# Kernel tuning notes

Hardware: AMD Instinct MI355X
Metric: run time of the kernel (lower is better)

## Reference

```python
import jax, jax.numpy as jnp
import numpy as np

H = 1024
V = 32000
S = 2048


def _lstm_cell(x, h_prev, c_prev, W_ih, W_hh, b_ih, b_hh):
    # PyTorch gate order: input, forget, cell(g), output
    gates = x @ W_ih.T + b_ih + h_prev @ W_hh.T + b_hh  # (1, 4H)
    i, f, g, o = jnp.split(gates, 4, axis=-1)
    i = jax.nn.sigmoid(i)
    f = jax.nn.sigmoid(f)
    g = jnp.tanh(g)
    o = jax.nn.sigmoid(o)
    c_new = f * c_prev + i * g
    h_new = o * jnp.tanh(c_new)
    return h_new, c_new


def setup_inputs() -> dict:
    key = jax.random.key(0)
    ks = jax.random.split(key, 16)
    sc = 0.05
    inp = {
        "input_ids": jax.random.randint(ks[0], (1,), 0, V, dtype=jnp.int64) if jax.config.jax_enable_x64 else jax.random.randint(ks[0], (1,), 0, V, dtype=jnp.int32),
        "h": jax.random.normal(ks[1], (2, 1, H), jnp.float32),
        "c": jax.random.normal(ks[2], (2, 1, H), jnp.float32),
        "encoder_outputs": jax.random.normal(ks[3], (S, H), jnp.float32),
        "embedding": jax.random.normal(ks[4], (V, H), jnp.float32) * sc,
        "W_ih0": jax.random.normal(ks[5], (4 * H, H), jnp.float32) * sc,
        "W_hh0": jax.random.normal(ks[6], (4 * H, H), jnp.float32) * sc,
        "b_ih0": jax.random.normal(ks[7], (4 * H,), jnp.float32) * sc,
        "b_hh0": jax.random.normal(ks[8], (4 * H,), jnp.float32) * sc,
        "W_ih1": jax.random.normal(ks[9], (4 * H, H), jnp.float32) * sc,
        "W_hh1": jax.random.normal(ks[10], (4 * H, H), jnp.float32) * sc,
        "b_ih1": jax.random.normal(ks[11], (4 * H,), jnp.float32) * sc,
        "b_hh1": jax.random.normal(ks[12], (4 * H,), jnp.float32) * sc,
        "W_out": jax.random.normal(ks[13], (V, H), jnp.float32) * sc,
        "b_out": jax.random.normal(ks[14], (V,), jnp.float32) * sc,
    }
    return inp


def reference(input_ids, h, c, encoder_outputs, embedding,
              W_ih0, W_hh0, b_ih0, b_hh0,
              W_ih1, W_hh1, b_ih1, b_hh1,
              W_out, b_out):
    # embedding lookup; dropout is identity in eval mode
    x = embedding[input_ids[0]][None, :]                      # (1, H)

    # attention: scores against layer-0 hidden state
    scores = encoder_outputs @ h[0, 0]                        # (S,)
    attn_w = jax.nn.softmax(scores)                           # (S,)
    ctx = attn_w @ encoder_outputs                            # (H,) attention_applied
    ctx_h = ctx[None, :]                                      # (1, H)

    # custom hidden-state injection: both layers' h replaced by context
    h0, c0 = _lstm_cell(x, ctx_h, c[0], W_ih0, W_hh0, b_ih0, b_hh0)
    h1, c1 = _lstm_cell(h0, ctx_h, c[1], W_ih1, W_hh1, b_ih1, b_hh1)

    logits = h1 @ W_out.T + b_out                             # (1, V)
    h_new = jnp.stack([h0, h1])                               # (2, 1, H)
    c_new = jnp.stack([c0, c1])                               # (2, 1, H)
    return logits, h_new, c_new, attn_w[None, :]
```

## Files before the change

### kernel.cpp

```cpp
#include <hip/hip_runtime.h>

#define HH 1024
#define VV 32000
#define SS 2048

__device__ __forceinline__ float wave_sum64(float v) {
    #pragma unroll
    for (int off = 32; off; off >>= 1) v += __shfl_down(v, off, 64);
    return v;
}

__global__ __launch_bounds__(256) void scores_kernel(
    const float* __restrict__ E, const float* __restrict__ h,
    float* __restrict__ scores) {
    int wave = (blockIdx.x * blockDim.x + threadIdx.x) >> 6;
    int lane = threadIdx.x & 63;
    const float4* Er = (const float4*)(E + (size_t)wave * HH);
    const float4* hv = (const float4*)h;
    float acc = 0.f;
    #pragma unroll
    for (int k = 0; k < 4; ++k) {
        float4 e = Er[lane + 64 * k];
        float4 x = hv[lane + 64 * k];
        acc += e.x * x.x + e.y * x.y + e.z * x.z + e.w * x.w;
    }
    acc = wave_sum64(acc);
    if (lane == 0) scores[wave] = acc;
}

__global__ __launch_bounds__(1024) void softmax_kernel(
    const float* __restrict__ scores,
    float* __restrict__ attn_ws, float* __restrict__ attn_out,
    float* __restrict__ ctx_acc) {
    __shared__ float red[16];
    __shared__ float s_max, s_sum;
    int t = threadIdx.x;
    float s0 = scores[t], s1 = scores[t + 1024];
    float m = fmaxf(s0, s1);
    #pragma unroll
    for (int off = 32; off; off >>= 1) m = fmaxf(m, __shfl_xor(m, off, 64));
    if ((t & 63) == 0) red[t >> 6] = m;
    __syncthreads();
    if (t == 0) {
        float v = red[0];
        #pragma unroll
        for (int i = 1; i < 16; ++i) v = fmaxf(v, red[i]);
        s_max = v;
    }
    __syncthreads();
    float e0 = expf(s0 - s_max), e1 = expf(s1 - s_max);
    float sum = e0 + e1;
    sum = wave_sum64(sum);
    if ((t & 63) == 0) red[t >> 6] = sum;
    __syncthreads();
    if (t == 0) {
        float v = 0.f;
        #pragma unroll
        for (int i = 0; i < 16; ++i) v += red[i];
        s_sum = v;
    }
    __syncthreads();
    float inv = 1.f / s_sum;
    float a0 = e0 * inv, a1 = e1 * inv;
    attn_ws[t] = a0;  attn_ws[t + 1024] = a1;
    attn_out[t] = a0; attn_out[t + 1024] = a1;
    ctx_acc[t] = 0.f;
}

__global__ __launch_bounds__(256) void ctx_kernel(
    const float* __restrict__ E, const float* __restrict__ attn,
    float* __restrict__ ctx_acc) {
    int t = threadIdx.x;
    int rowBase = blockIdx.x * 16;
    float4 acc = make_float4(0.f, 0.f, 0.f, 0.f);
    #pragma unroll
    for (int s = 0; s < 16; ++s) {
        float w = attn[rowBase + s];
        float4 e = ((const float4*)(E + (size_t)(rowBase + s) * HH))[t];
        acc.x += w * e.x; acc.y += w * e.y; acc.z += w * e.z; acc.w += w * e.w;
    }
    atomicAdd(&ctx_acc[4 * t + 0], acc.x);
    atomicAdd(&ctx_acc[4 * t + 1], acc.y);
    atomicAdd(&ctx_acc[4 * t + 2], acc.z);
    atomicAdd(&ctx_acc[4 * t + 3], acc.w);
}

__global__ __launch_bounds__(256) void gates_kernel(
    const float* __restrict__ Wih, const float* __restrict__ Whh,
    const float* __restrict__ bih, const float* __restrict__ bhh,
    const float* __restrict__ xin, const float* __restrict__ emb,
    const int* __restrict__ ids,
    const float* __restrict__ hprev, float* __restrict__ gates) {
    int wave = (blockIdx.x * blockDim.x + threadIdx.x) >> 6;
    int lane = threadIdx.x & 63;
    const float* x = (ids != nullptr) ? (emb + (size_t)ids[0] * HH) : xin;
    const float4* A  = (const float4*)(Wih + (size_t)wave * HH);
    const float4* B  = (const float4*)(Whh + (size_t)wave * HH);
    const float4* xv = (const float4*)x;
    const float4* hv = (const float4*)hprev;
    float acc = 0.f;
    #pragma unroll
    for (int k = 0; k < 4; ++k) {
        float4 a  = A[lane + 64 * k];
        float4 xx = xv[lane + 64 * k];
        acc += a.x * xx.x + a.y * xx.y + a.z * xx.z + a.w * xx.w;
        float4 b  = B[lane + 64 * k];
        float4 hh = hv[lane + 64 * k];
        acc += b.x * hh.x + b.y * hh.y + b.z * hh.z + b.w * hh.w;
    }
    acc = wave_sum64(acc);
    if (lane == 0) gates[wave] = acc + bih[wave] + bhh[wave];
}

__global__ __launch_bounds__(256) void lstm_elem_kernel(
    const float* __restrict__ gates, const float* __restrict__ c_prev,
    float* __restrict__ h_ws, float* __restrict__ c_ws,
    float* __restrict__ h_out, float* __restrict__ c_out) {
    int j = blockIdx.x * blockDim.x + threadIdx.x;
    float gi = gates[j];
    float gf = gates[j + 1024];
    float gg = gates[j + 2048];
    float go = gates[j + 3072];
    gi = 1.f / (1.f + expf(-gi));
    gf = 1.f / (1.f + expf(-gf));
    go = 1.f / (1.f + expf(-go));
    gg = tanhf(gg);
    float c = gf * c_prev[j] + gi * gg;
    float h = go * tanhf(c);
    h_ws[j] = h; c_ws[j] = c;
    h_out[j] = h; c_out[j] = c;
}

__global__ __launch_bounds__(256) void logits_kernel(
    const float* __restrict__ W, const float* __restrict__ b,
    const float* __restrict__ h, float* __restrict__ out) {
    int wave = (blockIdx.x * blockDim.x + threadIdx.x) >> 6;
    int lane = threadIdx.x & 63;
    const float4* Wr = (const float4*)(W + (size_t)wave * HH);
    const float4* hv = (const float4*)h;
    float acc = 0.f;
    #pragma unroll
    for (int k = 0; k < 4; ++k) {
        float4 w = Wr[lane + 64 * k];
        float4 x = hv[lane + 64 * k];
        acc += w.x * x.x + w.y * x.y + w.z * x.z + w.w * x.w;
    }
    acc = wave_sum64(acc);
    if (lane == 0) out[wave] = acc + b[wave];
}

extern "C" void kernel_launch(void* const* d_in, const int* in_sizes, int n_in,
                              void* d_out, int out_size, void* d_ws, size_t ws_size,
                              hipStream_t stream) {
    const int*   ids   = (const int*)  d_in[0];
    const float* h_in  = (const float*)d_in[1];
    const float* c_in  = (const float*)d_in[2];
    const float* E     = (const float*)d_in[3];
    const float* emb   = (const float*)d_in[4];
    const float* Wih0  = (const float*)d_in[5];
    const float* Whh0  = (const float*)d_in[6];
    const float* bih0  = (const float*)d_in[7];
    const float* bhh0  = (const float*)d_in[8];
    const float* Wih1  = (const float*)d_in[9];
    const float* Whh1  = (const float*)d_in[10];
    const float* bih1  = (const float*)d_in[11];
    const float* bhh1  = (const float*)d_in[12];
    const float* Wout  = (const float*)d_in[13];
    const float* bout  = (const float*)d_in[14];

    float* out = (float*)d_out;
    float* logits   = out;
    float* h0_out   = out + 32000;
    float* h1_out   = out + 32000 + 1024;
    float* c0_out   = out + 34048;
    float* c1_out   = out + 34048 + 1024;
    float* attn_out = out + 36096;

    float* ws = (float*)d_ws;
    float* scores  = ws;
    float* attn_ws = ws + 2048;
    float* ctx     = ws + 4096;
    float* gates0  = ws + 5120;
    float* gates1  = ws + 9216;
    float* h0_ws   = ws + 13312;
    float* c0_ws   = ws + 14336;
    float* h1_ws   = ws + 15360;
    float* c1_ws   = ws + 16384;

    scores_kernel<<<512, 256, 0, stream>>>(E, h_in, scores);
    softmax_kernel<<<1, 1024, 0, stream>>>(scores, attn_ws, attn_out, ctx);
    ctx_kernel<<<128, 256, 0, stream>>>(E, attn_ws, ctx);
    gates_kernel<<<1024, 256, 0, stream>>>(Wih0, Whh0, bih0, bhh0,
                                           nullptr, emb, ids, ctx, gates0);
    lstm_elem_kernel<<<4, 256, 0, stream>>>(gates0, c_in, h0_ws, c0_ws, h0_out, c0_out);
    gates_kernel<<<1024, 256, 0, stream>>>(Wih1, Whh1, bih1, bhh1,
                                           h0_ws, nullptr, nullptr, ctx, gates1);
    lstm_elem_kernel<<<4, 256, 0, stream>>>(gates1, c_in + 1024, h1_ws, c1_ws, h1_out, c1_out);
    logits_kernel<<<8000, 256, 0, stream>>>(Wout, bout, h1_ws, logits);
}
```

Measured before the change: 64.49 us.

## Fuse softmax into ctx and LSTM elementwise into following GEMVs

```diff
diff --git a/kernel.cpp b/kernel.cpp
--- a/kernel.cpp
+++ b/kernel.cpp
@@ -10,11 +10,18 @@
     return v;
 }
 
+__device__ __forceinline__ float sigmoidf(float x) {
+    return 1.f / (1.f + expf(-x));
+}
+
 __global__ __launch_bounds__(256) void scores_kernel(
     const float* __restrict__ E, const float* __restrict__ h,
-    float* __restrict__ scores) {
+    float* __restrict__ scores, float* __restrict__ ctx) {
     int wave = (blockIdx.x * blockDim.x + threadIdx.x) >> 6;
     int lane = threadIdx.x & 63;
+    if (blockIdx.x == 0) {
+        ((float4*)ctx)[threadIdx.x] = make_float4(0.f, 0.f, 0.f, 0.f);
+    }
     const float4* Er = (const float4*)(E + (size_t)wave * HH);
     const float4* hv = (const float4*)h;
     float acc = 0.f;
@@ -28,125 +35,171 @@
     if (lane == 0) scores[wave] = acc;
 }
 
-__global__ __launch_bounds__(1024) void softmax_kernel(
-    const float* __restrict__ scores,
-    float* __restrict__ attn_ws, float* __restrict__ attn_out,
-    float* __restrict__ ctx_acc) {
-    __shared__ float red[16];
+__global__ __launch_bounds__(256) void softmax_ctx_kernel(
+    const float* __restrict__ E, const float* __restrict__ scores,
+    float* __restrict__ attn_out, float* __restrict__ ctx) {
+    __shared__ float red[4];
     __shared__ float s_max, s_sum;
+    __shared__ float w[16];
     int t = threadIdx.x;
-    float s0 = scores[t], s1 = scores[t + 1024];
-    float m = fmaxf(s0, s1);
+    float4 a = ((const float4*)scores)[t];
+    float4 b = ((const float4*)scores)[t + 256];
+    float m = fmaxf(fmaxf(fmaxf(a.x, a.y), fmaxf(a.z, a.w)),
+                    fmaxf(fmaxf(b.x, b.y), fmaxf(b.z, b.w)));
     #pragma unroll
     for (int off = 32; off; off >>= 1) m = fmaxf(m, __shfl_xor(m, off, 64));
     if ((t & 63) == 0) red[t >> 6] = m;
     __syncthreads();
-    if (t == 0) {
-        float v = red[0];
-        #pragma unroll
-        for (int i = 1; i < 16; ++i) v = fmaxf(v, red[i]);
-        s_max = v;
-    }
-    __syncthreads();
-    float e0 = expf(s0 - s_max), e1 = expf(s1 - s_max);
-    float sum = e0 + e1;
+    if (t == 0) s_max = fmaxf(fmaxf(red[0], red[1]), fmaxf(red[2], red[3]));
+    __syncthreads();
+    float sm = s_max;
+    float sum = expf(a.x - sm) + expf(a.y - sm) + expf(a.z - sm) + expf(a.w - sm)
+              + expf(b.x - sm) + expf(b.y - sm) + expf(b.z - sm) + expf(b.w - sm);
     sum = wave_sum64(sum);
     if ((t & 63) == 0) red[t >> 6] = sum;
     __syncthreads();
-    if (t == 0) {
-        float v = 0.f;
-        #pragma unroll
-        for (int i = 0; i < 16; ++i) v += red[i];
-        s_sum = v;
-    }
+    if (t == 0) s_sum = red[0] + red[1] + red[2] + red[3];
     __syncthreads();
     float inv = 1.f / s_sum;
-    float a0 = e0 * inv, a1 = e1 * inv;
-    attn_ws[t] = a0;  attn_ws[t + 1024] = a1;
-    attn_out[t] = a0; attn_out[t + 1024] = a1;
-    ctx_acc[t] = 0.f;
-}
-
-__global__ __launch_bounds__(256) void ctx_kernel(
-    const float* __restrict__ E, const float* __restrict__ attn,
-    float* __restrict__ ctx_acc) {
-    int t = threadIdx.x;
     int rowBase = blockIdx.x * 16;
+    if (t < 16) {
+        float aw = expf(scores[rowBase + t] - sm) * inv;
+        w[t] = aw;
+        attn_out[rowBase + t] = aw;
+    }
+    __syncthreads();
     float4 acc = make_float4(0.f, 0.f, 0.f, 0.f);
     #pragma unroll
     for (int s = 0; s < 16; ++s) {
-        float w = attn[rowBase + s];
+        float ws_ = w[s];
         float4 e = ((const float4*)(E + (size_t)(rowBase + s) * HH))[t];
-        acc.x += w * e.x; acc.y += w * e.y; acc.z += w * e.z; acc.w += w * e.w;
-    }
-    atomicAdd(&ctx_acc[4 * t + 0], acc.x);
-    atomicAdd(&ctx_acc[4 * t + 1], acc.y);
-    atomicAdd(&ctx_acc[4 * t + 2], acc.z);
-    atomicAdd(&ctx_acc[4 * t + 3], acc.w);
-}
-
-__global__ __launch_bounds__(256) void gates_kernel(
+        acc.x += ws_ * e.x; acc.y += ws_ * e.y; acc.z += ws_ * e.z; acc.w += ws_ * e.w;
+    }
+    atomicAdd(&ctx[4 * t + 0], acc.x);
+    atomicAdd(&ctx[4 * t + 1], acc.y);
+    atomicAdd(&ctx[4 * t + 2], acc.z);
+    atomicAdd(&ctx[4 * t + 3], acc.w);
+}
+
+__global__ __launch_bounds__(256) void gates0_kernel(
     const float* __restrict__ Wih, const float* __restrict__ Whh,
     const float* __restrict__ bih, const float* __restrict__ bhh,
-    const float* __restrict__ xin, const float* __restrict__ emb,
-    const int* __restrict__ ids,
-    const float* __restrict__ hprev, float* __restrict__ gates) {
+    const float* __restrict__ emb, const int* __restrict__ ids,
+    const float* __restrict__ ctx, float* __restrict__ gates) {
     int wave = (blockIdx.x * blockDim.x + threadIdx.x) >> 6;
     int lane = threadIdx.x & 63;
-    const float* x = (ids != nullptr) ? (emb + (size_t)ids[0] * HH) : xin;
+    const float* x = emb + (size_t)ids[0] * HH;
     const float4* A  = (const float4*)(Wih + (size_t)wave * HH);
     const float4* B  = (const float4*)(Whh + (size_t)wave * HH);
     const float4* xv = (const float4*)x;
-    const float4* hv = (const float4*)hprev;
-    float acc = 0.f;
-    #pragma unroll
-    for (int k = 0; k < 4; ++k) {
-        float4 a  = A[lane + 64 * k];
+    const float4* hv = (const float4*)ctx;
+    float acc = 0.f;
+    #pragma unroll
+    for (int k = 0; k < 4; ++k) {
+        float4 aa = A[lane + 64 * k];
         float4 xx = xv[lane + 64 * k];
-        acc += a.x * xx.x + a.y * xx.y + a.z * xx.z + a.w * xx.w;
-        float4 b  = B[lane + 64 * k];
+        acc += aa.x * xx.x + aa.y * xx.y + aa.z * xx.z + aa.w * xx.w;
+        float4 bb = B[lane + 64 * k];
         float4 hh = hv[lane + 64 * k];
-        acc += b.x * hh.x + b.y * hh.y + b.z * hh.z + b.w * hh.w;
+        acc += bb.x * hh.x + bb.y * hh.y + bb.z * hh.z + bb.w * hh.w;
     }
     acc = wave_sum64(acc);
     if (lane == 0) gates[wave] = acc + bih[wave] + bhh[wave];
 }
 
-__global__ __launch_bounds__(256) void lstm_elem_kernel(
-    const float* __restrict__ gates, const float* __restrict__ c_prev,
-    float* __restrict__ h_ws, float* __restrict__ c_ws,
-    float* __restrict__ h_out, float* __restrict__ c_out) {
-    int j = blockIdx.x * blockDim.x + threadIdx.x;
-    float gi = gates[j];
-    float gf = gates[j + 1024];
-    float gg = gates[j + 2048];
-    float go = gates[j + 3072];
-    gi = 1.f / (1.f + expf(-gi));
-    gf = 1.f / (1.f + expf(-gf));
-    go = 1.f / (1.f + expf(-go));
-    gg = tanhf(gg);
-    float c = gf * c_prev[j] + gi * gg;
-    float h = go * tanhf(c);
-    h_ws[j] = h; c_ws[j] = c;
-    h_out[j] = h; c_out[j] = c;
-}
-
-__global__ __launch_bounds__(256) void logits_kernel(
-    const float* __restrict__ W, const float* __restrict__ b,
-    const float* __restrict__ h, float* __restrict__ out) {
-    int wave = (blockIdx.x * blockDim.x + threadIdx.x) >> 6;
-    int lane = threadIdx.x & 63;
-    const float4* Wr = (const float4*)(W + (size_t)wave * HH);
-    const float4* hv = (const float4*)h;
-    float acc = 0.f;
-    #pragma unroll
-    for (int k = 0; k < 4; ++k) {
-        float4 w = Wr[lane + 64 * k];
-        float4 x = hv[lane + 64 * k];
-        acc += w.x * x.x + w.y * x.y + w.z * x.z + w.w * x.w;
-    }
-    acc = wave_sum64(acc);
-    if (lane == 0) out[wave] = acc + b[wave];
+__global__ __launch_bounds__(256) void lstm1_gates_kernel(
+    const float* __restrict__ Wih, const float* __restrict__ Whh,
+    const float* __restrict__ bih, const float* __restrict__ bhh,
+    const float* __restrict__ gates0, const float* __restrict__ c0_in,
+    const float* __restrict__ ctx,
+    float* __restrict__ h0_out, float* __restrict__ c0_out,
+    float* __restrict__ gates1) {
+    __shared__ float4 hs[256];
+    int t = threadIdx.x;
+    {
+        float4 gi = ((const float4*)(gates0       ))[t];
+        float4 gf = ((const float4*)(gates0 + 1024))[t];
+        float4 gg = ((const float4*)(gates0 + 2048))[t];
+        float4 go = ((const float4*)(gates0 + 3072))[t];
+        float4 cp = ((const float4*)c0_in)[t];
+        float4 c4, h4;
+        c4.x = sigmoidf(gf.x) * cp.x + sigmoidf(gi.x) * tanhf(gg.x);
+        c4.y = sigmoidf(gf.y) * cp.y + sigmoidf(gi.y) * tanhf(gg.y);
+        c4.z = sigmoidf(gf.z) * cp.z + sigmoidf(gi.z) * tanhf(gg.z);
+        c4.w = sigmoidf(gf.w) * cp.w + sigmoidf(gi.w) * tanhf(gg.w);
+        h4.x = sigmoidf(go.x) * tanhf(c4.x);
+        h4.y = sigmoidf(go.y) * tanhf(c4.y);
+        h4.z = sigmoidf(go.z) * tanhf(c4.z);
+        h4.w = sigmoidf(go.w) * tanhf(c4.w);
+        hs[t] = h4;
+        if (blockIdx.x == 0) {
+            ((float4*)h0_out)[t] = h4;
+            ((float4*)c0_out)[t] = c4;
+        }
+    }
+    __syncthreads();
+    int row  = blockIdx.x * 4 + (t >> 6);
+    int lane = t & 63;
+    const float4* A  = (const float4*)(Wih + (size_t)row * HH);
+    const float4* B  = (const float4*)(Whh + (size_t)row * HH);
+    const float4* hv = (const float4*)hs;
+    const float4* cv = (const float4*)ctx;
+    float acc = 0.f;
+    #pragma unroll
+    for (int k = 0; k < 4; ++k) {
+        float4 aa = A[lane + 64 * k];
+        float4 xx = hv[lane + 64 * k];
+        acc += aa.x * xx.x + aa.y * xx.y + aa.z * xx.z + aa.w * xx.w;
+        float4 bb = B[lane + 64 * k];
+        float4 hh = cv[lane + 64 * k];
+        acc += bb.x * hh.x + bb.y * hh.y + bb.z * hh.z + bb.w * hh.w;
+    }
+    acc = wave_sum64(acc);
+    if (lane == 0) gates1[row] = acc + bih[row] + bhh[row];
+}
+
+__global__ __launch_bounds__(256) void logits_fused_kernel(
+    const float* __restrict__ W, const float* __restrict__ bout,
+    const float* __restrict__ gates1, const float* __restrict__ c1_in,
+    float* __restrict__ h1_out, float* __restrict__ c1_out,
+    float* __restrict__ out) {
+    __shared__ float4 hs[256];
+    int t = threadIdx.x;
+    {
+        float4 gi = ((const float4*)(gates1       ))[t];
+        float4 gf = ((const float4*)(gates1 + 1024))[t];
+        float4 gg = ((const float4*)(gates1 + 2048))[t];
+        float4 go = ((const float4*)(gates1 + 3072))[t];
+        float4 cp = ((const float4*)c1_in)[t];
+        float4 c4, h4;
+        c4.x = sigmoidf(gf.x) * cp.x + sigmoidf(gi.x) * tanhf(gg.x);
+        c4.y = sigmoidf(gf.y) * cp.y + sigmoidf(gi.y) * tanhf(gg.y);
+        c4.z = sigmoidf(gf.z) * cp.z + sigmoidf(gi.z) * tanhf(gg.z);
+        c4.w = sigmoidf(gf.w) * cp.w + sigmoidf(gi.w) * tanhf(gg.w);
+        h4.x = sigmoidf(go.x) * tanhf(c4.x);
+        h4.y = sigmoidf(go.y) * tanhf(c4.y);
+        h4.z = sigmoidf(go.z) * tanhf(c4.z);
+        h4.w = sigmoidf(go.w) * tanhf(c4.w);
+        hs[t] = h4;
+        if (blockIdx.x == 0) {
+            ((float4*)h1_out)[t] = h4;
+            ((float4*)c1_out)[t] = c4;
+        }
+    }
+    __syncthreads();
+    int row  = blockIdx.x * 4 + (t >> 6);
+    int lane = t & 63;
+    const float4* Wr = (const float4*)(W + (size_t)row * HH);
+    const float4* hv = (const float4*)hs;
+    float acc = 0.f;
+    #pragma unroll
+    for (int k = 0; k < 4; ++k) {
+        float4 w4 = Wr[lane + 64 * k];
+        float4 x4 = hv[lane + 64 * k];
+        acc += w4.x * x4.x + w4.y * x4.y + w4.z * x4.z + w4.w * x4.w;
+    }
+    acc = wave_sum64(acc);
+    if (lane == 0) out[row] = acc + bout[row];
 }
 
 extern "C" void kernel_launch(void* const* d_in, const int* in_sizes, int n_in,
@@ -171,30 +224,24 @@
     float* out = (float*)d_out;
     float* logits   = out;
     float* h0_out   = out + 32000;
-    float* h1_out   = out + 32000 + 1024;
+    float* h1_out   = out + 33024;
     float* c0_out   = out + 34048;
-    float* c1_out   = out + 34048 + 1024;
+    float* c1_out   = out + 35072;
     float* attn_out = out + 36096;
 
     float* ws = (float*)d_ws;
     float* scores  = ws;
-    float* attn_ws = ws + 2048;
-    float* ctx     = ws + 4096;
-    float* gates0  = ws + 5120;
-    float* gates1  = ws + 9216;
-    float* h0_ws   = ws + 13312;
-    float* c0_ws   = ws + 14336;
-    float* h1_ws   = ws + 15360;
-    float* c1_ws   = ws + 16384;
-
-    scores_kernel<<<512, 256, 0, stream>>>(E, h_in, scores);
-    softmax_kernel<<<1, 1024, 0, stream>>>(scores, attn_ws, attn_out, ctx);
-    ctx_kernel<<<128, 256, 0, stream>>>(E, attn_ws, ctx);
-    gates_kernel<<<1024, 256, 0, stream>>>(Wih0, Whh0, bih0, bhh0,
-                                           nullptr, emb, ids, ctx, gates0);
-    lstm_elem_kernel<<<4, 256, 0, stream>>>(gates0, c_in, h0_ws, c0_ws, h0_out, c0_out);
-    gates_kernel<<<1024, 256, 0, stream>>>(Wih1, Whh1, bih1, bhh1,
-                                           h0_ws, nullptr, nullptr, ctx, gates1);
-    lstm_elem_kernel<<<4, 256, 0, stream>>>(gates1, c_in + 1024, h1_ws, c1_ws, h1_out, c1_out);
-    logits_kernel<<<8000, 256, 0, stream>>>(Wout, bout, h1_ws, logits);
-}
+    float* ctx     = ws + 2048;
+    float* gates0  = ws + 3072;
+    float* gates1  = ws + 7168;
+
+    scores_kernel<<<512, 256, 0, stream>>>(E, h_in, scores, ctx);
+    softmax_ctx_kernel<<<128, 256, 0, stream>>>(E, scores, attn_out, ctx);
+    gates0_kernel<<<1024, 256, 0, stream>>>(Wih0, Whh0, bih0, bhh0,
+                                            emb, ids, ctx, gates0);
+    lstm1_gates_kernel<<<1024, 256, 0, stream>>>(Wih1, Whh1, bih1, bhh1,
+                                                 gates0, c_in, ctx,
+                                                 h0_out, c0_out, gates1);
+    logits_fused_kernel<<<8000, 256, 0, stream>>>(Wout, bout, gates1, c_in + 1024,
+                                                  h1_out, c1_out, logits);
+}
```

After: 68.99 us. 7.0% more time.
